# Kernel optimization log

Hardware: AMD Instinct MI355X
Metric: run time of the kernel (lower is better)

Reference implementation:

```python
import jax, jax.numpy as jnp
import numpy as np

N_PROBLEMS = 50000
N_HIDDEN = 128
B, T = 32, 1024


def setup_inputs() -> dict:
    key = jax.random.key(0)
    k1, k2, k3, k4, k5 = jax.random.split(key, 5)
    y = jax.random.uniform(k1, (B, T), dtype=jnp.float32)
    problem_seq = jax.random.randint(k2, (B, T), 0, N_PROBLEMS)
    embd_weight = jax.random.normal(k3, (N_PROBLEMS, N_HIDDEN), dtype=jnp.float32)
    lam_w = jax.random.normal(k4, (N_HIDDEN, 1), dtype=jnp.float32) * (1.0 / np.sqrt(N_HIDDEN))
    lam_b = jax.random.normal(k5, (1,), dtype=jnp.float32) * 0.01
    return {"y": y, "problem_seq": problem_seq, "embd_weight": embd_weight,
            "lam_w": lam_w, "lam_b": lam_b}


def reference(y, problem_seq, embd_weight, lam_w, lam_b):
    # x: [B, t, h] embedded problem sequence
    x = embd_weight[problem_seq]
    # cosine-similarity matrix between timesteps: [B, t, t]
    mag = jnp.linalg.norm(embd_weight, axis=1)[problem_seq]      # [B, t]
    denom = mag[:, :, None] * mag[:, None, :]                    # [B, t, t]
    sim = jnp.einsum('bth,bsh->bts', x, x) / denom
    sim = (sim + 1.0) * 0.5
    t = sim.shape[1]
    # strictly-lower-triangular causal mask (tril with diagonal=-1)
    mask = jnp.tril(jnp.ones((t, t), dtype=sim.dtype), k=-1)
    sim = sim * mask
    # reversed cumsum over key axis (time-since accumulation)
    delta_t = jax.lax.cumsum(sim, axis=2, reverse=True)
    # per-query decay rate lambda: [B, t, 1]
    lam = jnp.exp(x @ lam_w + lam_b)
    weight = sim * jnp.exp(-lam * delta_t)
    weight_normed = weight / (weight.sum(axis=2, keepdims=True) + 1e-6)
    yhat = jnp.einsum('bs,bts->bt', y, weight_normed)
    return jnp.clip(yhat, 0.01, 0.99)
```

## Files before the change

### kernel.cpp

```cpp
#include <hip/hip_runtime.h>
#include <math.h>

#define BB 32
#define TT 1024
#define HH 128

typedef __attribute__((ext_vector_type(8))) short short8;
typedef __attribute__((ext_vector_type(4))) float floatx4;

__device__ __forceinline__ unsigned short f2bf(float f) {
    unsigned u = __float_as_uint(f);
    u += 0x7fffu + ((u >> 16) & 1u);
    return (unsigned short)(u >> 16);
}

__global__ __launch_bounds__(256)
void gather_norm(const int* __restrict__ seq,
                 const float* __restrict__ embd,
                 const float* __restrict__ lam_w,
                 const float* __restrict__ lam_b,
                 unsigned short* __restrict__ xbf,
                 float* __restrict__ lam) {
    const int lane = threadIdx.x & 63;
    const int half = lane >> 5;
    const int l32  = lane & 31;
    const int row  = blockIdx.x * 8 + (threadIdx.x >> 6) * 2 + half;
    const int idx  = seq[row];
    float4 v = ((const float4*)(embd + (size_t)idx * HH))[l32];
    float4 w = ((const float4*)lam_w)[l32];
    float ss = v.x * v.x + v.y * v.y + v.z * v.z + v.w * v.w;
    float dw = v.x * w.x + v.y * w.y + v.z * w.z + v.w * w.w;
    #pragma unroll
    for (int off = 16; off > 0; off >>= 1) {
        ss += __shfl_xor(ss, off);
        dw += __shfl_xor(dw, off);
    }
    float inv = 1.0f / sqrtf(ss);
    unsigned b0 = f2bf(v.x * inv), b1 = f2bf(v.y * inv);
    unsigned b2 = f2bf(v.z * inv), b3 = f2bf(v.w * inv);
    uint2 o; o.x = b0 | (b1 << 16); o.y = b2 | (b3 << 16);
    ((uint2*)(xbf + (size_t)row * HH))[l32] = o;
    if (l32 == 0) lam[row] = expf(dw + lam_b[0]);
}

__device__ __forceinline__ void tile_part(const floatx4& acc, int s0, int t,
                                          float lmt, const float4& yv,
                                          float& S, float& W, float& Y) {
    float v0 = (s0 + 0 < t) ? (acc[0] + 1.f) * 0.5f : 0.f;
    float v1 = (s0 + 1 < t) ? (acc[1] + 1.f) * 0.5f : 0.f;
    float v2 = (s0 + 2 < t) ? (acc[2] + 1.f) * 0.5f : 0.f;
    float v3 = (s0 + 3 < t) ? (acc[3] + 1.f) * 0.5f : 0.f;
    float suf3 = v3;
    float suf2 = v2 + suf3;
    float suf1 = v1 + suf2;
    float suf0 = v0 + suf1;
    float e0 = __expf(-lmt * suf0);
    float e1 = __expf(-lmt * suf1);
    float e2 = __expf(-lmt * suf2);
    float e3 = __expf(-lmt * suf3);
    float w0 = v0 * e0, w1 = v1 * e1, w2 = v2 * e2, w3 = v3 * e3;
    S = suf0;
    W = (w0 + w1) + (w2 + w3);
    Y = (w0 * yv.x + w1 * yv.y) + (w2 * yv.z + w3 * yv.w);
}

__device__ __forceinline__ void resolve(float S, float W, float Y, float lmt,
                                        int tl, int quad,
                                        float& above, float& wl, float& yl) {
    float q0 = __shfl(S, tl);
    float q1 = __shfl(S, tl + 16);
    float q2 = __shfl(S, tl + 32);
    float q3 = __shfl(S, tl + 48);
    float tT = (q0 + q1) + (q2 + q3);
    float hq = (quad < 1 ? q1 : 0.f) + (quad < 2 ? q2 : 0.f) +
               (quad < 3 ? q3 : 0.f);
    float sc = __expf(-lmt * (above + hq));
    wl += W * sc;
    yl += Y * sc;
    above += tT;
}

__global__ __launch_bounds__(256, 4)
void sim_fused(const unsigned short* __restrict__ xbf,
               const float* __restrict__ lam,
               const float* __restrict__ y,
               float* __restrict__ out) {
    const int b    = blockIdx.x & 31;
    const int u    = 31 - (blockIdx.x >> 5);
    const int tid  = threadIdx.x;
    const int w    = tid >> 6;
    const int lane = tid & 63;
    const int tl   = lane & 15;
    const int quad = lane >> 4;

    const size_t rowbase = (size_t)b * TT;
    const int t0 = u * 32 + tl;
    const int t1 = t0 + 16;
    const float lam0 = lam[rowbase + t0];
    const float lam1 = lam[rowbase + t1];
    const float* yb = y + rowbase;

    __shared__ float Wc[4][2][16], Yc[4][2][16], Tc[4][2][16];

    short8 bq0[4], bq1[4];
    const short8* q0r = (const short8*)(xbf + (rowbase + t0) * HH);
    const short8* q1r = (const short8*)(xbf + (rowbase + t1) * HH);
    #pragma unroll
    for (int kk = 0; kk < 4; kk++) {
        bq0[kk] = q0r[kk * 4 + quad];
        bq1[kk] = q1r[kk * 4 + quad];
    }

    const int nst = 2 * u + 2;
    const int qn = nst >> 2, rem = nst & 3;
    const int cnt   = qn + (w < rem ? 1 : 0);
    const int start = w * qn + (w < rem ? w : rem);

    float wl0 = 0.f, yl0 = 0.f, above0 = 0.f;
    float wl1 = 0.f, yl1 = 0.f, above1 = 0.f;

    const int nsb = (cnt + 1) >> 1;
    for (int sb = nsb - 1; sb >= 0; --sb) {
        const int jA = start + 2 * sb;
        const int jB = jA + 1;
        const bool vB = (2 * sb + 1) < cnt;
        const int sbaseA = jA << 4;
        const int sbaseB = vB ? (jB << 4) : 0;

        const short8* arA = (const short8*)(xbf + (rowbase + sbaseA + tl) * HH);
        const short8* arB = (const short8*)(xbf + (rowbase + sbaseB + tl) * HH);
        short8 afA[4], afB[4];
        #pragma unroll
        for (int kk = 0; kk < 4; kk++) {
            afA[kk] = arA[kk * 4 + quad];
            afB[kk] = arB[kk * 4 + quad];
        }
        float4 yvA = ((const float4*)(yb + sbaseA))[quad];
        float4 yvB = ((const float4*)(yb + sbaseB))[quad];

        floatx4 aA0 = {0,0,0,0}, aA1 = {0,0,0,0};
        floatx4 aB0 = {0,0,0,0}, aB1 = {0,0,0,0};
        #pragma unroll
        for (int kk = 0; kk < 4; kk++) {
            aA0 = __builtin_amdgcn_mfma_f32_16x16x32_bf16(afA[kk], bq0[kk], aA0, 0, 0, 0);
            aA1 = __builtin_amdgcn_mfma_f32_16x16x32_bf16(afA[kk], bq1[kk], aA1, 0, 0, 0);
            aB0 = __builtin_amdgcn_mfma_f32_16x16x32_bf16(afB[kk], bq0[kk], aB0, 0, 0, 0);
            aB1 = __builtin_amdgcn_mfma_f32_16x16x32_bf16(afB[kk], bq1[kk], aB1, 0, 0, 0);
        }

        const int s0A = sbaseA + quad * 4;
        const int s0B = vB ? (sbaseB + quad * 4) : 0x40000000;

        float SB0, WB0, YB0, SB1, WB1, YB1;
        float SA0, WA0, YA0, SA1, WA1, YA1;
        tile_part(aB0, s0B, t0, lam0, yvB, SB0, WB0, YB0);
        tile_part(aB1, s0B, t1, lam1, yvB, SB1, WB1, YB1);
        tile_part(aA0, s0A, t0, lam0, yvA, SA0, WA0, YA0);
        tile_part(aA1, s0A, t1, lam1, yvA, SA1, WA1, YA1);

        resolve(SB0, WB0, YB0, lam0, tl, quad, above0, wl0, yl0);
        resolve(SB1, WB1, YB1, lam1, tl, quad, above1, wl1, yl1);
        resolve(SA0, WA0, YA0, lam0, tl, quad, above0, wl0, yl0);
        resolve(SA1, WA1, YA1, lam1, tl, quad, above1, wl1, yl1);
    }

    float Wt0 = __shfl(wl0, tl) + __shfl(wl0, tl + 16) +
                __shfl(wl0, tl + 32) + __shfl(wl0, tl + 48);
    float Yt0 = __shfl(yl0, tl) + __shfl(yl0, tl + 16) +
                __shfl(yl0, tl + 32) + __shfl(yl0, tl + 48);
    float Wt1 = __shfl(wl1, tl) + __shfl(wl1, tl + 16) +
                __shfl(wl1, tl + 32) + __shfl(wl1, tl + 48);
    float Yt1 = __shfl(yl1, tl) + __shfl(yl1, tl + 16) +
                __shfl(yl1, tl + 32) + __shfl(yl1, tl + 48);
    if (quad == 0) {
        Wc[w][0][tl] = Wt0; Yc[w][0][tl] = Yt0; Tc[w][0][tl] = above0;
        Wc[w][1][tl] = Wt1; Yc[w][1][tl] = Yt1; Tc[w][1][tl] = above1;
    }
    __syncthreads();

    if (tid < 32) {
        const int g = tid >> 4, l = tid & 15;
        const int t = u * 32 + g * 16 + l;
        const float lt = lam[rowbase + t];
        float A = 0.f, W = 0.f, Y = 0.f;
        #pragma unroll
        for (int ww = 3; ww >= 0; --ww) {
            float sc = __expf(-lt * A);
            W += Wc[ww][g][l] * sc;
            Y += Yc[ww][g][l] * sc;
            A += Tc[ww][g][l];
        }
        float r = Y / (W + 1e-6f);
        out[rowbase + t] = fminf(fmaxf(r, 0.01f), 0.99f);
    }
}

extern "C" void kernel_launch(void* const* d_in, const int* in_sizes, int n_in,
                              void* d_out, int out_size, void* d_ws, size_t ws_size,
                              hipStream_t stream) {
    const float* y     = (const float*)d_in[0];
    const int*   seq   = (const int*)  d_in[1];
    const float* embd  = (const float*)d_in[2];
    const float* lam_w = (const float*)d_in[3];
    const float* lam_b = (const float*)d_in[4];
    float* out = (float*)d_out;

    unsigned short* xbf = (unsigned short*)d_ws;
    float* lam = (float*)(xbf + (size_t)BB * TT * HH);

    gather_norm<<<BB * TT / 8, 256, 0, stream>>>(seq, embd, lam_w, lam_b, xbf, lam);
    sim_fused<<<BB * 32, 256, 0, stream>>>(xbf, lam, y, out);
}
```

Measured before the change: 104.6 us.

## Double-buffer key-tile register loads across superblocks in sim_fused

Restructures the main loop of sim_fused into a two-stage software pipeline. Each iteration prefetches the next superblock's bf16 key fragments and y values into a second register buffer while the MFMAs and exp-based reductions run on the current one. Out-of-range superblocks are clamped for loading and fully masked in compute, so an odd count costs one wasted masked iteration. The extra live registers lead the launch bounds to drop from 4 to 3 waves-per-SIMD occupancy. This trades latency hiding across waves for explicit prefetch within each wave.

```diff
diff --git a/kernel.cpp b/kernel.cpp
--- a/kernel.cpp
+++ b/kernel.cpp
@@ -80,7 +80,64 @@
     above += tT;
 }
 
-__global__ __launch_bounds__(256, 4)
+__device__ __forceinline__ void issue_loads(const unsigned short* __restrict__ xbf,
+                                            const float* __restrict__ yb,
+                                            size_t rowbase, int tl, int quad,
+                                            int start, int cnt, int sb,
+                                            short8 a[8], float4& yA, float4& yB) {
+    int jA = start + 2 * sb;
+    if (jA < 0) jA = 0;
+    const bool vB = (2 * sb + 1) < cnt && sb >= 0;
+    const int sbaseA = jA << 4;
+    const int sbaseB = vB ? ((jA + 1) << 4) : sbaseA;
+    const short8* arA = (const short8*)(xbf + (rowbase + sbaseA + tl) * HH);
+    const short8* arB = (const short8*)(xbf + (rowbase + sbaseB + tl) * HH);
+    #pragma unroll
+    for (int kk = 0; kk < 4; kk++) {
+        a[kk]     = arA[kk * 4 + quad];
+        a[4 + kk] = arB[kk * 4 + quad];
+    }
+    yA = ((const float4*)(yb + sbaseA))[quad];
+    yB = ((const float4*)(yb + sbaseB))[quad];
+}
+
+__device__ __forceinline__ void compute_sb(int sb, int start, int cnt,
+                                           const short8 a[8],
+                                           const short8 bq0[4], const short8 bq1[4],
+                                           const float4& yA, const float4& yB,
+                                           int t0, int t1, float lam0, float lam1,
+                                           int tl, int quad,
+                                           float& above0, float& wl0, float& yl0,
+                                           float& above1, float& wl1, float& yl1) {
+    const bool vA = (2 * sb)     < cnt && sb >= 0;
+    const bool vB = (2 * sb + 1) < cnt && sb >= 0;
+    const int jA = start + 2 * sb;
+    floatx4 aA0 = {0,0,0,0}, aA1 = {0,0,0,0};
+    floatx4 aB0 = {0,0,0,0}, aB1 = {0,0,0,0};
+    #pragma unroll
+    for (int kk = 0; kk < 4; kk++) {
+        aA0 = __builtin_amdgcn_mfma_f32_16x16x32_bf16(a[kk],     bq0[kk], aA0, 0, 0, 0);
+        aA1 = __builtin_amdgcn_mfma_f32_16x16x32_bf16(a[kk],     bq1[kk], aA1, 0, 0, 0);
+        aB0 = __builtin_amdgcn_mfma_f32_16x16x32_bf16(a[4 + kk], bq0[kk], aB0, 0, 0, 0);
+        aB1 = __builtin_amdgcn_mfma_f32_16x16x32_bf16(a[4 + kk], bq1[kk], aB1, 0, 0, 0);
+    }
+    const int s0A = vA ? ((jA << 4) + quad * 4)       : 0x40000000;
+    const int s0B = vB ? (((jA + 1) << 4) + quad * 4) : 0x40000000;
+
+    float SB0, WB0, YB0, SB1, WB1, YB1;
+    float SA0, WA0, YA0, SA1, WA1, YA1;
+    tile_part(aB0, s0B, t0, lam0, yB, SB0, WB0, YB0);
+    tile_part(aB1, s0B, t1, lam1, yB, SB1, WB1, YB1);
+    tile_part(aA0, s0A, t0, lam0, yA, SA0, WA0, YA0);
+    tile_part(aA1, s0A, t1, lam1, yA, SA1, WA1, YA1);
+
+    resolve(SB0, WB0, YB0, lam0, tl, quad, above0, wl0, yl0);
+    resolve(SB1, WB1, YB1, lam1, tl, quad, above1, wl1, yl1);
+    resolve(SA0, WA0, YA0, lam0, tl, quad, above0, wl0, yl0);
+    resolve(SA1, WA1, YA1, lam1, tl, quad, above1, wl1, yl1);
+}
+
+__global__ __launch_bounds__(256, 3)
 void sim_fused(const unsigned short* __restrict__ xbf,
                const float* __restrict__ lam,
                const float* __restrict__ y,
@@ -120,48 +177,23 @@
     float wl1 = 0.f, yl1 = 0.f, above1 = 0.f;
 
     const int nsb = (cnt + 1) >> 1;
-    for (int sb = nsb - 1; sb >= 0; --sb) {
-        const int jA = start + 2 * sb;
-        const int jB = jA + 1;
-        const bool vB = (2 * sb + 1) < cnt;
-        const int sbaseA = jA << 4;
-        const int sbaseB = vB ? (jB << 4) : 0;
-
-        const short8* arA = (const short8*)(xbf + (rowbase + sbaseA + tl) * HH);
-        const short8* arB = (const short8*)(xbf + (rowbase + sbaseB + tl) * HH);
-        short8 afA[4], afB[4];
-        #pragma unroll
-        for (int kk = 0; kk < 4; kk++) {
-            afA[kk] = arA[kk * 4 + quad];
-            afB[kk] = arB[kk * 4 + quad];
-        }
-        float4 yvA = ((const float4*)(yb + sbaseA))[quad];
-        float4 yvB = ((const float4*)(yb + sbaseB))[quad];
-
-        floatx4 aA0 = {0,0,0,0}, aA1 = {0,0,0,0};
-        floatx4 aB0 = {0,0,0,0}, aB1 = {0,0,0,0};
-        #pragma unroll
-        for (int kk = 0; kk < 4; kk++) {
-            aA0 = __builtin_amdgcn_mfma_f32_16x16x32_bf16(afA[kk], bq0[kk], aA0, 0, 0, 0);
-            aA1 = __builtin_amdgcn_mfma_f32_16x16x32_bf16(afA[kk], bq1[kk], aA1, 0, 0, 0);
-            aB0 = __builtin_amdgcn_mfma_f32_16x16x32_bf16(afB[kk], bq0[kk], aB0, 0, 0, 0);
-            aB1 = __builtin_amdgcn_mfma_f32_16x16x32_bf16(afB[kk], bq1[kk], aB1, 0, 0, 0);
-        }
-
-        const int s0A = sbaseA + quad * 4;
-        const int s0B = vB ? (sbaseB + quad * 4) : 0x40000000;
-
-        float SB0, WB0, YB0, SB1, WB1, YB1;
-        float SA0, WA0, YA0, SA1, WA1, YA1;
-        tile_part(aB0, s0B, t0, lam0, yvB, SB0, WB0, YB0);
-        tile_part(aB1, s0B, t1, lam1, yvB, SB1, WB1, YB1);
-        tile_part(aA0, s0A, t0, lam0, yvA, SA0, WA0, YA0);
-        tile_part(aA1, s0A, t1, lam1, yvA, SA1, WA1, YA1);
-
-        resolve(SB0, WB0, YB0, lam0, tl, quad, above0, wl0, yl0);
-        resolve(SB1, WB1, YB1, lam1, tl, quad, above1, wl1, yl1);
-        resolve(SA0, WA0, YA0, lam0, tl, quad, above0, wl0, yl0);
-        resolve(SA1, WA1, YA1, lam1, tl, quad, above1, wl1, yl1);
+
+    short8 abuf0[8], abuf1[8];
+    float4 y0A, y0B, y1A, y1B;
+
+    int sb = nsb - 1;
+    issue_loads(xbf, yb, rowbase, tl, quad, start, cnt, sb, abuf0, y0A, y0B);
+    for (; sb >= 0; sb -= 2) {
+        issue_loads(xbf, yb, rowbase, tl, quad, start, cnt, sb - 1,
+                    abuf1, y1A, y1B);
+        compute_sb(sb, start, cnt, abuf0, bq0, bq1, y0A, y0B,
+                   t0, t1, lam0, lam1, tl, quad,
+                   above0, wl0, yl0, above1, wl1, yl1);
+        issue_loads(xbf, yb, rowbase, tl, quad, start, cnt, sb - 2,
+                    abuf0, y0A, y0B);
+        compute_sb(sb - 1, start, cnt, abuf1, bq0, bq1, y1A, y1B,
+                   t0, t1, lam0, lam1, tl, quad,
+                   above0, wl0, yl0, above1, wl1, yl1);
     }
 
     float Wt0 = __shfl(wl0, tl) + __shfl(wl0, tl + 16) +
```

Result: slower. 108.1 us (+3.4%).

## Split each query tile's key range across two blocks and merge partials

Applied to the files above, without the earlier changes.

Each block's key-tile range is divided into two halves handled by separate blocks, which doubles the grid to 2048 blocks and gives better load balance across CUs. Each half writes partial weighted sums and the total similarity mass to workspace, and a new merge kernel combines them with the decay correction exp(-lam*T), then normalises and clips. This adds a third kernel launch and a small round trip through global memory.

```diff
diff --git a/kernel.cpp b/kernel.cpp
--- a/kernel.cpp
+++ b/kernel.cpp
@@ -81,12 +81,16 @@
 }
 
 __global__ __launch_bounds__(256, 4)
-void sim_fused(const unsigned short* __restrict__ xbf,
-               const float* __restrict__ lam,
-               const float* __restrict__ y,
-               float* __restrict__ out) {
+void sim_half(const unsigned short* __restrict__ xbf,
+              const float* __restrict__ lam,
+              const float* __restrict__ y,
+              float* __restrict__ Wp,
+              float* __restrict__ Yp,
+              float* __restrict__ Tp) {
     const int b    = blockIdx.x & 31;
-    const int u    = 31 - (blockIdx.x >> 5);
+    const int r    = blockIdx.x >> 5;
+    const int u    = 31 - (r >> 1);
+    const int half = r & 1;
     const int tid  = threadIdx.x;
     const int w    = tid >> 6;
     const int lane = tid & 63;
@@ -111,21 +115,21 @@
         bq1[kk] = q1r[kk * 4 + quad];
     }
 
-    const int nst = 2 * u + 2;
-    const int qn = nst >> 2, rem = nst & 3;
+    const int ntile = u + 1;
+    const int base_tile = half * ntile;
+    const int qn = ntile >> 2, rem = ntile & 3;
     const int cnt   = qn + (w < rem ? 1 : 0);
-    const int start = w * qn + (w < rem ? w : rem);
-
-    float wl0 = 0.f, yl0 = 0.f, above0 = 0.f;
-    float wl1 = 0.f, yl1 = 0.f, above1 = 0.f;
+    const int start = base_tile + w * qn + (w < rem ? w : rem);
+
+    float wl0 = 0.f, yl0 = 0.f, run0 = 0.f;
+    float wl1 = 0.f, yl1 = 0.f, run1 = 0.f;
 
     const int nsb = (cnt + 1) >> 1;
     for (int sb = nsb - 1; sb >= 0; --sb) {
         const int jA = start + 2 * sb;
-        const int jB = jA + 1;
         const bool vB = (2 * sb + 1) < cnt;
         const int sbaseA = jA << 4;
-        const int sbaseB = vB ? (jB << 4) : 0;
+        const int sbaseB = vB ? ((jA + 1) << 4) : sbaseA;
 
         const short8* arA = (const short8*)(xbf + (rowbase + sbaseA + tl) * HH);
         const short8* arB = (const short8*)(xbf + (rowbase + sbaseB + tl) * HH);
@@ -158,10 +162,10 @@
         tile_part(aA0, s0A, t0, lam0, yvA, SA0, WA0, YA0);
         tile_part(aA1, s0A, t1, lam1, yvA, SA1, WA1, YA1);
 
-        resolve(SB0, WB0, YB0, lam0, tl, quad, above0, wl0, yl0);
-        resolve(SB1, WB1, YB1, lam1, tl, quad, above1, wl1, yl1);
-        resolve(SA0, WA0, YA0, lam0, tl, quad, above0, wl0, yl0);
-        resolve(SA1, WA1, YA1, lam1, tl, quad, above1, wl1, yl1);
+        resolve(SB0, WB0, YB0, lam0, tl, quad, run0, wl0, yl0);
+        resolve(SB1, WB1, YB1, lam1, tl, quad, run1, wl1, yl1);
+        resolve(SA0, WA0, YA0, lam0, tl, quad, run0, wl0, yl0);
+        resolve(SA1, WA1, YA1, lam1, tl, quad, run1, wl1, yl1);
     }
 
     float Wt0 = __shfl(wl0, tl) + __shfl(wl0, tl + 16) +
@@ -173,8 +177,8 @@
     float Yt1 = __shfl(yl1, tl) + __shfl(yl1, tl + 16) +
                 __shfl(yl1, tl + 32) + __shfl(yl1, tl + 48);
     if (quad == 0) {
-        Wc[w][0][tl] = Wt0; Yc[w][0][tl] = Yt0; Tc[w][0][tl] = above0;
-        Wc[w][1][tl] = Wt1; Yc[w][1][tl] = Yt1; Tc[w][1][tl] = above1;
+        Wc[w][0][tl] = Wt0; Yc[w][0][tl] = Yt0; Tc[w][0][tl] = run0;
+        Wc[w][1][tl] = Wt1; Yc[w][1][tl] = Yt1; Tc[w][1][tl] = run1;
     }
     __syncthreads();
 
@@ -190,9 +194,29 @@
             Y += Yc[ww][g][l] * sc;
             A += Tc[ww][g][l];
         }
-        float r = Y / (W + 1e-6f);
-        out[rowbase + t] = fminf(fmaxf(r, 0.01f), 0.99f);
-    }
+        const int p = (b * 64 + u * 2 + half) * 32 + tid;
+        Wp[p] = W; Yp[p] = Y; Tp[p] = A;
+    }
+}
+
+__global__ __launch_bounds__(256)
+void merge2(const float* __restrict__ Wp,
+            const float* __restrict__ Yp,
+            const float* __restrict__ Tp,
+            const float* __restrict__ lam,
+            float* __restrict__ out) {
+    const int id   = blockIdx.x * 256 + threadIdx.x;
+    const int tcol = id & 31;
+    const int u    = (id >> 5) & 31;
+    const int b    = id >> 10;
+    const int t    = u * 32 + tcol;
+    const float lt = lam[b * TT + t];
+    const int p0 = (b * 64 + u * 2) * 32 + tcol;
+    const int p1 = p0 + 32;
+    float W = Wp[p1] + __expf(-lt * Tp[p1]) * Wp[p0];
+    float Y = Yp[p1] + __expf(-lt * Tp[p1]) * Yp[p0];
+    float r = Y / (W + 1e-6f);
+    out[b * TT + t] = fminf(fmaxf(r, 0.01f), 0.99f);
 }
 
 extern "C" void kernel_launch(void* const* d_in, const int* in_sizes, int n_in,
@@ -207,7 +231,11 @@
 
     unsigned short* xbf = (unsigned short*)d_ws;
     float* lam = (float*)(xbf + (size_t)BB * TT * HH);
+    float* Wp  = lam + BB * TT;
+    float* Yp  = Wp + BB * 64 * 32;
+    float* Tp  = Yp + BB * 64 * 32;
 
     gather_norm<<<BB * TT / 8, 256, 0, stream>>>(seq, embd, lam_w, lam_b, xbf, lam);
-    sim_fused<<<BB * 32, 256, 0, stream>>>(xbf, lam, y, out);
-}
+    sim_half<<<BB * 64, 256, 0, stream>>>(xbf, lam, y, Wp, Yp, Tp);
+    merge2<<<BB * TT / 256, 256, 0, stream>>>(Wp, Yp, Tp, lam, out);
+}
```

New measurement: 110.6 us. 1.06x slower.
